# Kernel tuning notes

Hardware: AMD Instinct MI355X
Metric: run time of the kernel (lower is better)

## Reference

```python
import jax, jax.numpy as jnp
import numpy as np

D_MODEL = 2048
D_INNER = 4096  # d_model * expand_factor
LN_EPS = 1e-5


def setup_inputs() -> dict:
    key = jax.random.key(0)
    k1, k2, k3, k4 = jax.random.split(key, 4)
    B, S = 2, 4096
    x = jax.random.normal(k1, (B, S, D_MODEL), dtype=jnp.float32)
    gamma = jnp.ones((D_MODEL,), dtype=jnp.float32)
    beta = jnp.zeros((D_MODEL,), dtype=jnp.float32)
    # nn.Linear-like small init to keep activations in-range
    W_in = jax.random.normal(k2, (2 * D_INNER, D_MODEL), dtype=jnp.float32) * 0.02
    W_out = jax.random.normal(k3, (D_MODEL, D_INNER), dtype=jnp.float32) * 0.02
    dt_min, dt_max = 0.001, 0.1
    dt = jax.random.uniform(k4, (D_INNER,), dtype=jnp.float32) * (dt_max - dt_min) + dt_min
    return {"x": x, "gamma": gamma, "beta": beta, "W_in": W_in, "W_out": W_out, "dt": dt}


def reference(x, gamma, beta, W_in, W_out, dt):
    # x: [B, S, D_MODEL]
    identity = x
    # LayerNorm over last dim
    mu = jnp.mean(x, axis=-1, keepdims=True)
    var = jnp.mean(jnp.square(x - mu), axis=-1, keepdims=True)
    xn = (x - mu) * jax.lax.rsqrt(var + LN_EPS) * gamma + beta
    # in_proj: [B, S, 2*D_INNER]
    projected = jnp.einsum("bsd,ed->bse", xn, W_in)
    z, gate = jnp.split(projected, 2, axis=-1)
    # z gated by sigmoid of clamped z (clamp only inside sigmoid)
    z_gated = z * jax.nn.sigmoid(jnp.clip(z, -15.0, 15.0))
    # temporal weighting by softmax(-dt) over d_inner
    dt_weights = jax.nn.softmax(-dt)  # [D_INNER]
    z_temporal = z_gated * dt_weights  # broadcast over [B, S, D_INNER]
    # gate path: silu on clamped gate
    output = z_temporal * jax.nn.silu(jnp.clip(gate, -15.0, 15.0))
    # out_proj back to d_model
    output = jnp.einsum("bse,de->bsd", output, W_out)
    return output + identity
```

## Files before the change

### kernel.cpp

```cpp
#include <hip/hip_runtime.h>
#include <cstdint>
#include <cstddef>

#define T_TOK 8192
#define DM    2048
#define DI    4096
#define TWO_DI 8192

typedef __attribute__((ext_vector_type(8))) short bf16x8;
typedef __attribute__((ext_vector_type(4))) float f32x4;

__device__ __forceinline__ unsigned short f2bf(float f) {
  union { float f; unsigned u; } c; c.f = f;
  unsigned u = c.u;
  unsigned r = (u + 0x7fffu + ((u >> 16) & 1u)) >> 16;
  return (unsigned short)r;
}

__global__ __launch_bounds__(256) void ln_kernel(
    const float* __restrict__ x, const float* __restrict__ gamma,
    const float* __restrict__ beta, unsigned short* __restrict__ xn) {
  const int t = blockIdx.x;
  const int tid = threadIdx.x;
  const float* row = x + (size_t)t * DM;
  float4 v0 = reinterpret_cast<const float4*>(row)[tid];
  float4 v1 = reinterpret_cast<const float4*>(row)[tid + 256];
  float s  = v0.x + v0.y + v0.z + v0.w + v1.x + v1.y + v1.z + v1.w;
  float ss = v0.x*v0.x + v0.y*v0.y + v0.z*v0.z + v0.w*v0.w
           + v1.x*v1.x + v1.y*v1.y + v1.z*v1.z + v1.w*v1.w;
  #pragma unroll
  for (int off = 32; off > 0; off >>= 1) {
    s  += __shfl_down(s, off);
    ss += __shfl_down(ss, off);
  }
  __shared__ float red[8];
  __shared__ float mu_s, inv_s;
  if ((tid & 63) == 0) { red[tid >> 6] = s; red[4 + (tid >> 6)] = ss; }
  __syncthreads();
  if (tid == 0) {
    float S  = red[0] + red[1] + red[2] + red[3];
    float SS = red[4] + red[5] + red[6] + red[7];
    float mu  = S * (1.0f / DM);
    float var = SS * (1.0f / DM) - mu * mu;
    mu_s = mu;
    inv_s = rsqrtf(var + 1e-5f);
  }
  __syncthreads();
  const float mu = mu_s, inv = inv_s;
  float4 g0 = reinterpret_cast<const float4*>(gamma)[tid];
  float4 b0 = reinterpret_cast<const float4*>(beta)[tid];
  float4 g1 = reinterpret_cast<const float4*>(gamma)[tid + 256];
  float4 b1 = reinterpret_cast<const float4*>(beta)[tid + 256];
  ushort4 o0, o1;
  o0.x = f2bf((v0.x - mu) * inv * g0.x + b0.x);
  o0.y = f2bf((v0.y - mu) * inv * g0.y + b0.y);
  o0.z = f2bf((v0.z - mu) * inv * g0.z + b0.z);
  o0.w = f2bf((v0.w - mu) * inv * g0.w + b0.w);
  o1.x = f2bf((v1.x - mu) * inv * g1.x + b1.x);
  o1.y = f2bf((v1.y - mu) * inv * g1.y + b1.y);
  o1.z = f2bf((v1.z - mu) * inv * g1.z + b1.z);
  o1.w = f2bf((v1.w - mu) * inv * g1.w + b1.w);
  reinterpret_cast<ushort4*>(xn + (size_t)t * DM)[tid]       = o0;
  reinterpret_cast<ushort4*>(xn + (size_t)t * DM)[tid + 256] = o1;
}

__global__ __launch_bounds__(256) void cvt_both(
    const float* __restrict__ a, unsigned short* __restrict__ oa, int n4a,
    const float* __restrict__ b, unsigned short* __restrict__ ob, int n4b) {
  int i = blockIdx.x * 256 + threadIdx.x;
  const float* src;
  unsigned short* dst;
  int idx;
  if (i < n4a) { src = a; dst = oa; idx = i; }
  else { idx = i - n4a; if (idx >= n4b) return; src = b; dst = ob; }
  float4 v = reinterpret_cast<const float4*>(src)[idx];
  ushort4 o;
  o.x = f2bf(v.x); o.y = f2bf(v.y); o.z = f2bf(v.z); o.w = f2bf(v.w);
  reinterpret_cast<ushort4*>(dst)[idx] = o;
}

__global__ __launch_bounds__(256) void dt_softmax(
    const float* __restrict__ dt, float* __restrict__ w) {
  const int tid = threadIdx.x;
  float e[16];
  float local = 0.f;
  #pragma unroll
  for (int i = 0; i < 16; ++i) {
    float v = __expf(-dt[i * 256 + tid]);
    e[i] = v;
    local += v;
  }
  #pragma unroll
  for (int off = 32; off > 0; off >>= 1) local += __shfl_down(local, off);
  __shared__ float red[4];
  __shared__ float tot;
  if ((tid & 63) == 0) red[tid >> 6] = local;
  __syncthreads();
  if (tid == 0) tot = red[0] + red[1] + red[2] + red[3];
  __syncthreads();
  const float inv = 1.f / tot;
  #pragma unroll
  for (int i = 0; i < 16; ++i) w[i * 256 + tid] = e[i] * inv;
}

__device__ __forceinline__ float actf(float z, float g, float w) {
  float zc = fminf(fmaxf(z, -15.f), 15.f);
  float sz = 1.f / (1.f + __expf(-zc));
  float gc = fminf(fmaxf(g, -15.f), 15.f);
  float sg = 1.f / (1.f + __expf(-gc));
  return z * sz * w * gc * sg;
}

#define BAR()    __builtin_amdgcn_s_barrier()
#define SCHED0() __builtin_amdgcn_sched_barrier(0)
#define PRIO1()  __builtin_amdgcn_s_setprio(1)
#define PRIO0()  __builtin_amdgcn_s_setprio(0)
#define WAIT_LGKM0() asm volatile("s_waitcnt lgkmcnt(0)" ::: "memory")
#define WAIT_VM4()   asm volatile("s_waitcnt vmcnt(4)" ::: "memory")

#define GLD16(gaddr, laddr) __builtin_amdgcn_global_load_lds(                 \
    (const __attribute__((address_space(1))) void*)(gaddr),                   \
    (__attribute__((address_space(3))) void*)(laddr), 16, 0, 0)

#define STAGE(ldsbase, gb, k0) do {                                           \
    GLD16((gb) + sOff  + (k0), &(ldsbase)[tid * 8]);                          \
    GLD16((gb) + sOff2 + (k0), &(ldsbase)[tid * 8 + 4096]);                   \
  } while (0)

#define G1_NKT 32
#define G1_NIT 16

__global__ __launch_bounds__(512, 2) void gemm1_fused8(
    const unsigned short* __restrict__ A, const unsigned short* __restrict__ W,
    const float* __restrict__ dtw, unsigned short* __restrict__ act) {
  __shared__ unsigned short lA [2][256 * 64];
  __shared__ unsigned short lB1[2][128 * 64];
  __shared__ unsigned short lB2[2][128 * 64];

  const int tid  = threadIdx.x;
  const int lane = tid & 63;
  const int wmI  = (tid >> 6) >> 2;
  const int wnI  = (tid >> 6) & 3;
  const int tM = blockIdx.y * 256;
  const int tN = blockIdx.x * 128;

  const int r0   = lane & 15;
  const int hi4  = lane >> 4;
  const int swz0 = (hi4 ^ (r0 & 7)) << 3;
  const int swz1 = swz0 ^ 32;
  const int aRow = (wmI * 128 + r0) * 64;
  const int bRow = (wnI * 32  + r0) * 64;

  const int srow = tid >> 3;
  const int scol = ((tid & 7) ^ (srow & 7)) << 3;
  const size_t sOff  = (size_t)srow * DM + scol;
  const size_t sOff2 = sOff + (size_t)64 * DM;

  const unsigned short* Ab    = A + (size_t)tM * DM;
  const unsigned short* Ab128 = Ab + (size_t)128 * DM;
  const unsigned short* B1b   = W + (size_t)tN * DM;
  const unsigned short* B2b   = W + (size_t)(tN + DI) * DM;

  f32x4 accZ[8][2], accG[8][2];
  #pragma unroll
  for (int i = 0; i < 8; ++i)
    #pragma unroll
    for (int j = 0; j < 2; ++j) {
      accZ[i][j] = f32x4{0.f, 0.f, 0.f, 0.f};
      accG[i][j] = f32x4{0.f, 0.f, 0.f, 0.f};
    }
  bf16x8 aR[4], bR1[2], bR2[2];

#define G1_LDA(b, idx, sw) do {                                               \
    _Pragma("unroll") for (int i = 0; i < 4; ++i)                             \
      aR[i] = *reinterpret_cast<const bf16x8*>(                               \
          &lA[b][aRow + ((idx) + i) * 1024 + (sw)]);                          \
  } while (0)
#define G1_LDB(b, sw) do {                                                    \
    _Pragma("unroll") for (int j = 0; j < 2; ++j) {                           \
      bR1[j] = *reinterpret_cast<const bf16x8*>(&lB1[b][bRow + j*1024 + (sw)]); \
      bR2[j] = *reinterpret_cast<const bf16x8*>(&lB2[b][bRow + j*1024 + (sw)]); \
    }                                                                         \
  } while (0)
#define G1_MFMA16(ib) do {                                                    \
    _Pragma("unroll") for (int i = 0; i < 4; ++i)                             \
      _Pragma("unroll") for (int j = 0; j < 2; ++j) {                         \
        accZ[(ib)+i][j] = __builtin_amdgcn_mfma_f32_16x16x32_bf16(            \
            aR[i], bR1[j], accZ[(ib)+i][j], 0, 0, 0);                         \
        accG[(ib)+i][j] = __builtin_amdgcn_mfma_f32_16x16x32_bf16(            \
            aR[i], bR2[j], accG[(ib)+i][j], 0, 0, 0);                         \
      }                                                                       \
  } while (0)
#define G1_TAIL() do {                                                        \
    BAR(); WAIT_LGKM0(); SCHED0();                                            \
  } while (0)
#define G1_MF(ib) do {                                                        \
    PRIO1(); G1_MFMA16(ib); PRIO0(); SCHED0(); BAR();                         \
  } while (0)

  STAGE(lA[0],        Ab,    0);
  STAGE(&lA[0][8192], Ab128, 0);
  STAGE(lB1[0],       B1b,   0);
  STAGE(lB2[0],       B2b,   0);
  STAGE(lB1[1],       B1b,   64);
  STAGE(lB2[1],       B2b,   64);
  WAIT_VM4();
  BAR();

  #pragma unroll 1
  for (int t = 0; t < G1_NIT; ++t) {
    const int k1  = (2 * t + 1) * 64;
    const int kt2 = 2 * t + 2;
    const int kt3 = 2 * t + 3;
    const int k2 = (kt2 < G1_NKT ? kt2 : G1_NKT - 1) * 64;
    const int k3 = (kt3 < G1_NKT ? kt3 : G1_NKT - 1) * 64;

    G1_LDA(0, 0, swz0); G1_LDB(0, swz0);
    STAGE(lA[1], Ab, k1); STAGE(&lA[1][8192], Ab128, k1);
    G1_TAIL(); G1_MF(0);
    G1_LDA(0, 4, swz0);
    G1_TAIL(); G1_MF(4);
    G1_LDA(0, 0, swz1); G1_LDB(0, swz1);
    G1_TAIL(); G1_MF(0);
    G1_LDA(0, 4, swz1);
    STAGE(lB1[0], B1b, k2); STAGE(lB2[0], B2b, k2);
    WAIT_VM4();
    G1_TAIL(); G1_MF(4);

    G1_LDA(1, 0, swz0); G1_LDB(1, swz0);
    STAGE(lA[0], Ab, k2); STAGE(&lA[0][8192], Ab128, k2);
    G1_TAIL(); G1_MF(0);
    G1_LDA(1, 4, swz0);
    G1_TAIL(); G1_MF(4);
    G1_LDA(1, 0, swz1); G1_LDB(1, swz1);
    G1_TAIL(); G1_MF(0);
    G1_LDA(1, 4, swz1);
    STAGE(lB1[1], B1b, k3); STAGE(lB2[1], B2b, k3);
    WAIT_VM4();
    G1_TAIL(); G1_MF(4);
  }

  const int qr   = hi4 << 2;
  const int colb = tN + wnI * 32 + r0;
  const float w0 = dtw[colb];
  const float w1 = dtw[colb + 16];
  #pragma unroll
  for (int i = 0; i < 8; ++i) {
    #pragma unroll
    for (int r = 0; r < 4; ++r) {
      const size_t base = (size_t)(tM + wmI * 128 + i * 16 + qr + r) * DI + colb;
      act[base]      = f2bf(actf(accZ[i][0][r], accG[i][0][r], w0));
      act[base + 16] = f2bf(actf(accZ[i][1][r], accG[i][1][r], w1));
    }
  }
#undef G1_LDA
#undef G1_LDB
#undef G1_MFMA16
#undef G1_TAIL
#undef G1_MF
}

#define G2_NKT 64
#define G2_NIT 32

__global__ __launch_bounds__(512, 2) void gemm2_res8(
    const unsigned short* __restrict__ A, const unsigned short* __restrict__ Bm,
    float* __restrict__ out, const float* __restrict__ ident) {
  __shared__ unsigned short lA[2][256 * 64];
  __shared__ unsigned short lB[2][256 * 64];

  const int tid  = threadIdx.x;
  const int lane = tid & 63;
  const int wmI  = (tid >> 6) >> 2;
  const int wnI  = (tid >> 6) & 3;
  const int tM = blockIdx.y * 256;
  const int tN = blockIdx.x * 256;

  const int r0   = lane & 15;
  const int hi4  = lane >> 4;
  const int swz0 = (hi4 ^ (r0 & 7)) << 3;
  const int swz1 = swz0 ^ 32;
  const int aRow = (wmI * 128 + r0) * 64;
  const int bRow = (wnI * 64  + r0) * 64;

  const int srow = tid >> 3;
  const int scol = ((tid & 7) ^ (srow & 7)) << 3;
  const size_t sOff  = (size_t)srow * DI + scol;
  const size_t sOff2 = sOff + (size_t)64 * DI;

  const unsigned short* Ab    = A + (size_t)tM * DI;
  const unsigned short* Ab128 = Ab + (size_t)128 * DI;
  const unsigned short* Bb    = Bm + (size_t)tN * DI;
  const unsigned short* Bb128 = Bb + (size_t)128 * DI;

  f32x4 acc[8][4];
  #pragma unroll
  for (int i = 0; i < 8; ++i)
    #pragma unroll
    for (int j = 0; j < 4; ++j) acc[i][j] = f32x4{0.f, 0.f, 0.f, 0.f};
  bf16x8 aR[4], bR[4];

#define G2_LDA(b, idx, sw) do {                                               \
    _Pragma("unroll") for (int i = 0; i < 4; ++i)                             \
      aR[i] = *reinterpret_cast<const bf16x8*>(                               \
          &lA[b][aRow + ((idx) + i) * 1024 + (sw)]);                          \
  } while (0)
#define G2_LDB(b, sw) do {                                                    \
    _Pragma("unroll") for (int j = 0; j < 4; ++j)                             \
      bR[j] = *reinterpret_cast<const bf16x8*>(&lB[b][bRow + j*1024 + (sw)]); \
  } while (0)
#define G2_MFMA16(ib) do {                                                    \
    _Pragma("unroll") for (int i = 0; i < 4; ++i)                             \
      _Pragma("unroll") for (int j = 0; j < 4; ++j)                           \
        acc[(ib)+i][j] = __builtin_amdgcn_mfma_f32_16x16x32_bf16(             \
            aR[i], bR[j], acc[(ib)+i][j], 0, 0, 0);                           \
  } while (0)
#define G2_TAIL() do {                                                        \
    BAR(); WAIT_LGKM0(); SCHED0();                                            \
  } while (0)
#define G2_MF(ib) do {                                                        \
    PRIO1(); G2_MFMA16(ib); PRIO0(); SCHED0(); BAR();                         \
  } while (0)

  STAGE(lA[0],        Ab,    0);
  STAGE(&lA[0][8192], Ab128, 0);
  STAGE(lB[0],        Bb,    0);
  STAGE(&lB[0][8192], Bb128, 0);
  STAGE(lB[1],        Bb,    64);
  STAGE(&lB[1][8192], Bb128, 64);
  WAIT_VM4();
  BAR();

  #pragma unroll 1
  for (int t = 0; t < G2_NIT; ++t) {
    const int k1  = (2 * t + 1) * 64;
    const int kt2 = 2 * t + 2;
    const int kt3 = 2 * t + 3;
    const int k2 = (kt2 < G2_NKT ? kt2 : G2_NKT - 1) * 64;
    const int k3 = (kt3 < G2_NKT ? kt3 : G2_NKT - 1) * 64;

    G2_LDA(0, 0, swz0); G2_LDB(0, swz0);
    STAGE(lA[1], Ab, k1); STAGE(&lA[1][8192], Ab128, k1);
    G2_TAIL(); G2_MF(0);
    G2_LDA(0, 4, swz0);
    G2_TAIL(); G2_MF(4);
    G2_LDA(0, 0, swz1); G2_LDB(0, swz1);
    G2_TAIL(); G2_MF(0);
    G2_LDA(0, 4, swz1);
    STAGE(lB[0], Bb, k2); STAGE(&lB[0][8192], Bb128, k2);
    WAIT_VM4();
    G2_TAIL(); G2_MF(4);

    G2_LDA(1, 0, swz0); G2_LDB(1, swz0);
    STAGE(lA[0], Ab, k2); STAGE(&lA[0][8192], Ab128, k2);
    G2_TAIL(); G2_MF(0);
    G2_LDA(1, 4, swz0);
    G2_TAIL(); G2_MF(4);
    G2_LDA(1, 0, swz1); G2_LDB(1, swz1);
    G2_TAIL(); G2_MF(0);
    G2_LDA(1, 4, swz1);
    STAGE(lB[1], Bb, k3); STAGE(&lB[1][8192], Bb128, k3);
    WAIT_VM4();
    G2_TAIL(); G2_MF(4);
  }

  const int qr   = hi4 << 2;
  const int colb = tN + wnI * 64 + r0;
  #pragma unroll
  for (int i = 0; i < 8; ++i) {
    #pragma unroll
    for (int r = 0; r < 4; ++r) {
      const size_t rowoff = (size_t)(tM + wmI * 128 + i * 16 + qr + r) * DM;
      #pragma unroll
      for (int j = 0; j < 4; ++j) {
        const size_t idx = rowoff + colb + j * 16;
        out[idx] = acc[i][j][r] + ident[idx];
      }
    }
  }
#undef G2_LDA
#undef G2_LDB
#undef G2_MFMA16
#undef G2_TAIL
#undef G2_MF
}

extern "C" void kernel_launch(void* const* d_in, const int* in_sizes, int n_in,
                              void* d_out, int out_size, void* d_ws, size_t ws_size,
                              hipStream_t stream) {
  const float* x     = (const float*)d_in[0];
  const float* gamma = (const float*)d_in[1];
  const float* beta  = (const float*)d_in[2];
  const float* W_in  = (const float*)d_in[3];
  const float* W_out = (const float*)d_in[4];
  const float* dt    = (const float*)d_in[5];
  float* out = (float*)d_out;

  char* ws = (char*)d_ws;
  unsigned short* xn     = (unsigned short*)(ws);
  unsigned short* win_b  = (unsigned short*)(ws + ((size_t)32 << 20));
  unsigned short* wout_b = (unsigned short*)(ws + ((size_t)64 << 20));
  float*          dtw    = (float*)(ws + ((size_t)80 << 20));
  unsigned short* act    = (unsigned short*)(ws + ((size_t)96 << 20));

  const int n4_in  = TWO_DI * DM / 4;
  const int n4_out = DM * DI / 4;

  ln_kernel<<<T_TOK, 256, 0, stream>>>(x, gamma, beta, xn);
  cvt_both<<<(n4_in + n4_out + 255) / 256, 256, 0, stream>>>(
      W_in, win_b, n4_in, W_out, wout_b, n4_out);
  dt_softmax<<<1, 256, 0, stream>>>(dt, dtw);

  gemm1_fused8<<<dim3(DI / 128, T_TOK / 256), 512, 0, stream>>>(
      xn, win_b, dtw, act);

  gemm2_res8<<<dim3(DM / 256, T_TOK / 256), 512, 0, stream>>>(
      act, wout_b, out, x);
}
```

Before: 574.5 us.

## Replace tuned 256x256 pipelined out-projection GEMM with simple 128x128 single-buffered kernel

Swaps the hand-scheduled, double-buffered 256x256-tile out_proj GEMM, with its interleaved staging and MFMA priority hints, for a generic 128x128-tile kernel. The new kernel stages each K-slice directly into LDS with global_load_lds and runs 16 MFMAs per wave per 32-K step. It uses single buffering with two barriers per K iteration, so load and compute no longer overlap inside a block. The smaller tiles give more blocks and lower per-block register and LDS use, at the cost of more global traffic per FLOP.

```diff
diff --git a/kernel.cpp b/kernel.cpp
--- a/kernel.cpp
+++ b/kernel.cpp
@@ -260,129 +260,82 @@
 #undef G1_MF
 }
 
-#define G2_NKT 64
-#define G2_NIT 32
-
-__global__ __launch_bounds__(512, 2) void gemm2_res8(
+#define BM 128
+#define BN 128
+#define BK 64
+
+__global__ __launch_bounds__(256, 2) void gemm_nt_res(
     const unsigned short* __restrict__ A, const unsigned short* __restrict__ Bm,
-    float* __restrict__ out, const float* __restrict__ ident) {
-  __shared__ unsigned short lA[2][256 * 64];
-  __shared__ unsigned short lB[2][256 * 64];
-
+    float* __restrict__ Cf, const float* __restrict__ ident, int M, int N, int K) {
+  __shared__ unsigned short lA[BM * BK];
+  __shared__ unsigned short lB[BN * BK];
   const int tid  = threadIdx.x;
   const int lane = tid & 63;
-  const int wmI  = (tid >> 6) >> 2;
-  const int wnI  = (tid >> 6) & 3;
-  const int tM = blockIdx.y * 256;
-  const int tN = blockIdx.x * 256;
-
-  const int r0   = lane & 15;
-  const int hi4  = lane >> 4;
-  const int swz0 = (hi4 ^ (r0 & 7)) << 3;
-  const int swz1 = swz0 ^ 32;
-  const int aRow = (wmI * 128 + r0) * 64;
-  const int bRow = (wnI * 64  + r0) * 64;
-
-  const int srow = tid >> 3;
-  const int scol = ((tid & 7) ^ (srow & 7)) << 3;
-  const size_t sOff  = (size_t)srow * DI + scol;
-  const size_t sOff2 = sOff + (size_t)64 * DI;
-
-  const unsigned short* Ab    = A + (size_t)tM * DI;
-  const unsigned short* Ab128 = Ab + (size_t)128 * DI;
-  const unsigned short* Bb    = Bm + (size_t)tN * DI;
-  const unsigned short* Bb128 = Bb + (size_t)128 * DI;
-
-  f32x4 acc[8][4];
-  #pragma unroll
-  for (int i = 0; i < 8; ++i)
+  const int wave = tid >> 6;
+  const int wm = (wave >> 1) << 6;
+  const int wn = (wave & 1) << 6;
+  const int tM = blockIdx.y * BM;
+  const int tN = blockIdx.x * BN;
+
+  f32x4 acc[4][4];
+  #pragma unroll
+  for (int i = 0; i < 4; ++i)
     #pragma unroll
     for (int j = 0; j < 4; ++j) acc[i][j] = f32x4{0.f, 0.f, 0.f, 0.f};
-  bf16x8 aR[4], bR[4];
-
-#define G2_LDA(b, idx, sw) do {                                               \
-    _Pragma("unroll") for (int i = 0; i < 4; ++i)                             \
-      aR[i] = *reinterpret_cast<const bf16x8*>(                               \
-          &lA[b][aRow + ((idx) + i) * 1024 + (sw)]);                          \
-  } while (0)
-#define G2_LDB(b, sw) do {                                                    \
-    _Pragma("unroll") for (int j = 0; j < 4; ++j)                             \
-      bR[j] = *reinterpret_cast<const bf16x8*>(&lB[b][bRow + j*1024 + (sw)]); \
-  } while (0)
-#define G2_MFMA16(ib) do {                                                    \
-    _Pragma("unroll") for (int i = 0; i < 4; ++i)                             \
-      _Pragma("unroll") for (int j = 0; j < 4; ++j)                           \
-        acc[(ib)+i][j] = __builtin_amdgcn_mfma_f32_16x16x32_bf16(             \
-            aR[i], bR[j], acc[(ib)+i][j], 0, 0, 0);                           \
-  } while (0)
-#define G2_TAIL() do {                                                        \
-    BAR(); WAIT_LGKM0(); SCHED0();                                            \
-  } while (0)
-#define G2_MF(ib) do {                                                        \
-    PRIO1(); G2_MFMA16(ib); PRIO0(); SCHED0(); BAR();                         \
-  } while (0)
-
-  STAGE(lA[0],        Ab,    0);
-  STAGE(&lA[0][8192], Ab128, 0);
-  STAGE(lB[0],        Bb,    0);
-  STAGE(&lB[0][8192], Bb128, 0);
-  STAGE(lB[1],        Bb,    64);
-  STAGE(&lB[1][8192], Bb128, 64);
-  WAIT_VM4();
-  BAR();
-
-  #pragma unroll 1
-  for (int t = 0; t < G2_NIT; ++t) {
-    const int k1  = (2 * t + 1) * 64;
-    const int kt2 = 2 * t + 2;
-    const int kt3 = 2 * t + 3;
-    const int k2 = (kt2 < G2_NKT ? kt2 : G2_NKT - 1) * 64;
-    const int k3 = (kt3 < G2_NKT ? kt3 : G2_NKT - 1) * 64;
-
-    G2_LDA(0, 0, swz0); G2_LDB(0, swz0);
-    STAGE(lA[1], Ab, k1); STAGE(&lA[1][8192], Ab128, k1);
-    G2_TAIL(); G2_MF(0);
-    G2_LDA(0, 4, swz0);
-    G2_TAIL(); G2_MF(4);
-    G2_LDA(0, 0, swz1); G2_LDB(0, swz1);
-    G2_TAIL(); G2_MF(0);
-    G2_LDA(0, 4, swz1);
-    STAGE(lB[0], Bb, k2); STAGE(&lB[0][8192], Bb128, k2);
-    WAIT_VM4();
-    G2_TAIL(); G2_MF(4);
-
-    G2_LDA(1, 0, swz0); G2_LDB(1, swz0);
-    STAGE(lA[0], Ab, k2); STAGE(&lA[0][8192], Ab128, k2);
-    G2_TAIL(); G2_MF(0);
-    G2_LDA(1, 4, swz0);
-    G2_TAIL(); G2_MF(4);
-    G2_LDA(1, 0, swz1); G2_LDB(1, swz1);
-    G2_TAIL(); G2_MF(0);
-    G2_LDA(1, 4, swz1);
-    STAGE(lB[1], Bb, k3); STAGE(&lB[1][8192], Bb128, k3);
-    WAIT_VM4();
-    G2_TAIL(); G2_MF(4);
-  }
-
-  const int qr   = hi4 << 2;
-  const int colb = tN + wnI * 64 + r0;
-  #pragma unroll
-  for (int i = 0; i < 8; ++i) {
+
+  const unsigned short* Ab = A + (size_t)tM * K;
+  const unsigned short* Bb = Bm + (size_t)tN * K;
+
+  for (int k0 = 0; k0 < K; k0 += BK) {
+    #pragma unroll
+    for (int i = 0; i < 4; ++i) {
+      const int t8  = i * 256 + tid;
+      const int row = t8 >> 3;
+      const int s8  = t8 & 7;
+      const int col = ((s8 ^ (row & 7)) << 3);
+      __builtin_amdgcn_global_load_lds(
+          (const __attribute__((address_space(1))) void*)(Ab + (size_t)row * K + k0 + col),
+          (__attribute__((address_space(3))) void*)(&lA[t8 << 3]), 16, 0, 0);
+      __builtin_amdgcn_global_load_lds(
+          (const __attribute__((address_space(1))) void*)(Bb + (size_t)row * K + k0 + col),
+          (__attribute__((address_space(3))) void*)(&lB[t8 << 3]), 16, 0, 0);
+    }
+    __syncthreads();
+
+    #pragma unroll
+    for (int kk = 0; kk < BK; kk += 32) {
+      const int r0 = lane & 15;
+      const int s8 = (((kk >> 3) + (lane >> 4)) ^ (r0 & 7)) << 3;
+      bf16x8 af[4], bfr[4];
+      #pragma unroll
+      for (int i = 0; i < 4; ++i)
+        af[i] = *reinterpret_cast<const bf16x8*>(&lA[(wm + i * 16 + r0) * BK + s8]);
+      #pragma unroll
+      for (int j = 0; j < 4; ++j)
+        bfr[j] = *reinterpret_cast<const bf16x8*>(&lB[(wn + j * 16 + r0) * BK + s8]);
+      #pragma unroll
+      for (int i = 0; i < 4; ++i)
+        #pragma unroll
+        for (int j = 0; j < 4; ++j)
+          acc[i][j] = __builtin_amdgcn_mfma_f32_16x16x32_bf16(af[i], bfr[j], acc[i][j], 0, 0, 0);
+    }
+    __syncthreads();
+  }
+
+  const int cn = tN + wn + (lane & 15);
+  const int rm = tM + wm + ((lane >> 4) << 2);
+  #pragma unroll
+  for (int i = 0; i < 4; ++i) {
     #pragma unroll
     for (int r = 0; r < 4; ++r) {
-      const size_t rowoff = (size_t)(tM + wmI * 128 + i * 16 + qr + r) * DM;
+      const size_t rowoff = (size_t)(rm + i * 16 + r) * N;
       #pragma unroll
       for (int j = 0; j < 4; ++j) {
-        const size_t idx = rowoff + colb + j * 16;
-        out[idx] = acc[i][j][r] + ident[idx];
+        const size_t idx = rowoff + cn + j * 16;
+        Cf[idx] = acc[i][j][r] + ident[idx];
       }
     }
   }
-#undef G2_LDA
-#undef G2_LDB
-#undef G2_MFMA16
-#undef G2_TAIL
-#undef G2_MF
 }
 
 extern "C" void kernel_launch(void* const* d_in, const int* in_sizes, int n_in,
@@ -414,6 +367,6 @@
   gemm1_fused8<<<dim3(DI / 128, T_TOK / 256), 512, 0, stream>>>(
       xn, win_b, dtw, act);
 
-  gemm2_res8<<<dim3(DM / 256, T_TOK / 256), 512, 0, stream>>>(
-      act, wout_b, out, x);
-}
+  gemm_nt_res<<<dim3(DM / BN, T_TOK / BM), 256, 0, stream>>>(
+      act, wout_b, out, x, T_TOK, DM, DI);
+}
```

Measured after the change: 623.0 us. 1.08x slower.
